# Optimization experiments

Hardware: AMD Instinct MI355X
Metric: run time of the kernel (lower is better)

## Reference

```python
import jax, jax.numpy as jnp
import numpy as np

METRIC_SCALE = 0.01  # metric = I + 0.01 * outer(p, p)


def setup_inputs() -> dict:
    key = jax.random.key(0)
    kq, kk = jax.random.split(key)
    query_points = jax.random.normal(kq, (8192, 512), dtype=jnp.float32)
    key_points = jax.random.normal(kk, (8192, 512), dtype=jnp.float32)
    return {"query_points": query_points, "key_points": key_points}


def reference(query_points, key_points):
    # diff_ij = q_i - k_j;  dist^2 under metric (I + c * p p^T) is
    # ||diff||^2 + c * (p . diff)^2 -- avoids materializing [Nq, Nk, d] diffs.
    c = METRIC_SCALE
    qq = jnp.sum(query_points * query_points, axis=-1)          # [Nq]
    kk = jnp.sum(key_points * key_points, axis=-1)              # [Nk]
    qk = jnp.einsum('qd,kd->qk', query_points, key_points)      # [Nq, Nk]
    norm2 = jnp.maximum(qq[:, None] + kk[None, :] - 2.0 * qk, 0.0)
    qdot = qq[:, None] - qk                                     # q_i . (q_i - k_j)
    kdot = qk - kk[None, :]                                     # k_j . (q_i - k_j) (sign irrelevant, squared)
    query_dist = jnp.sqrt(norm2 + c * qdot * qdot)
    key_dist = jnp.sqrt(norm2 + c * kdot * kdot)
    scores = -0.5 * (query_dist + key_dist)
    return jax.nn.softmax(scores, axis=-1)
```

## Files before the change

### kernel.cpp

```cpp
#include <hip/hip_runtime.h>
#include <stdint.h>


#define NQ 8192
#define NK 8192
#define DIM 512
#define CSCALE 0.01f

typedef float f32x4 __attribute__((ext_vector_type(4)));
typedef short s16x8 __attribute__((ext_vector_type(8)));
typedef unsigned short u16x4 __attribute__((ext_vector_type(4)));

__device__ __forceinline__ unsigned short f2bf(float x) {
  union { float f; uint32_t u; } c; c.f = x;
  uint32_t u = c.u;
  return (unsigned short)((u + 0x7fffu + ((u >> 16) & 1u)) >> 16);
}

__device__ __forceinline__ float bf2f(unsigned short h) {
  union { uint32_t u; float f; } c; c.u = ((uint32_t)h) << 16;
  return c.f;
}

__device__ __forceinline__ s16x8 pack8(f32x4 a, f32x4 b) {
  s16x8 r;
  r[0]=(short)f2bf(a.x); r[1]=(short)f2bf(a.y);
  r[2]=(short)f2bf(a.z); r[3]=(short)f2bf(a.w);
  r[4]=(short)f2bf(b.x); r[5]=(short)f2bf(b.y);
  r[6]=(short)f2bf(b.z); r[7]=(short)f2bf(b.w);
  return r;
}

#define GLOAD_LDS16(g, l)                                                      \
  __builtin_amdgcn_global_load_lds(                                            \
      (const __attribute__((address_space(1))) void*)(g),                      \
      (__attribute__((address_space(3))) void*)(l), 16, 0, 0)

__global__ __launch_bounds__(256) void prep_full_kernel(
    const float* __restrict__ q, const float* __restrict__ k,
    unsigned short* __restrict__ qbf, unsigned short* __restrict__ kbf,
    float* __restrict__ qq, float* __restrict__ kk) {
  int rowg = blockIdx.x * 4 + (threadIdx.x >> 6);
  int lane = threadIdx.x & 63;
  const float* src; unsigned short* dst; float* nrm; int row;
  if (rowg < NQ) { src = q; dst = qbf; nrm = qq; row = rowg; }
  else           { src = k; dst = kbf; nrm = kk; row = rowg - NQ; }
  const float* p = src + (size_t)row * DIM + lane * 8;
  f32x4 a = *(const f32x4*)p;
  f32x4 b = *(const f32x4*)(p + 4);
  float ss = a.x*a.x + a.y*a.y + a.z*a.z + a.w*a.w
           + b.x*b.x + b.y*b.y + b.z*b.z + b.w*b.w;
  *(s16x8*)(dst + (size_t)row * DIM + lane * 8) = pack8(a, b);
#pragma unroll
  for (int mask = 1; mask < 64; mask <<= 1) ss += __shfl_xor(ss, mask, 64);
  if (lane == 0) nrm[row] = ss;
}

__global__ __launch_bounds__(256) void prep_norms_kernel(
    const float* __restrict__ q, const float* __restrict__ k,
    float* __restrict__ qq, float* __restrict__ kk) {
  int rowg = blockIdx.x * 4 + (threadIdx.x >> 6);
  int lane = threadIdx.x & 63;
  const float* src; float* nrm; int row;
  if (rowg < NQ) { src = q; nrm = qq; row = rowg; }
  else           { src = k; nrm = kk; row = rowg - NQ; }
  const float* p = src + (size_t)row * DIM + lane * 8;
  f32x4 a = *(const f32x4*)p;
  f32x4 b = *(const f32x4*)(p + 4);
  float ss = a.x*a.x + a.y*a.y + a.z*a.z + a.w*a.w
           + b.x*b.x + b.y*b.y + b.z*b.z + b.w*b.w;
#pragma unroll
  for (int mask = 1; mask < 64; mask <<= 1) ss += __shfl_xor(ss, mask, 64);
  if (lane == 0) nrm[row] = ss;
}

__device__ __forceinline__ float score_fn(float qkv, float qqv, float kkv) {
  float n2 = fmaxf(qqv + kkv - 2.f * qkv, 0.f);
  float qd = qqv - qkv;
  float kd = qkv - kkv;
  return -0.5f * (__builtin_amdgcn_sqrtf(n2 + CSCALE * qd * qd) +
                  __builtin_amdgcn_sqrtf(n2 + CSCALE * kd * kd));
}

__global__ __launch_bounds__(256) void gemm_exp_kernel(
    const unsigned short* __restrict__ qbf, const unsigned short* __restrict__ kbf,
    const float* __restrict__ qq, const float* __restrict__ kk,
    unsigned short* __restrict__ E) {
  __shared__ alignas(16) unsigned short smem[8192];
  const int tid = threadIdx.x;
  const int m0 = blockIdx.y * 128;
  const int n0 = blockIdx.x * 128;
  const int wave = tid >> 6, lane = tid & 63;
  const int wr = wave >> 1, wc = wave & 1;
  const int quad = lane >> 4, lcol = lane & 15;

  const int srow = tid >> 2;
  const int gsw = (tid & 3) ^ ((srow >> 1) & 3);
  const unsigned short* ga = qbf + (size_t)(m0 + srow) * DIM + gsw * 8;
  const unsigned short* gb = kbf + (size_t)(n0 + srow) * DIM + gsw * 8;
  char* la0 = (char*)smem + wave * 1024;
  char* lb0 = (char*)smem + 8192 + wave * 1024;

  f32x4 acc[4][4];
#pragma unroll
  for (int mi = 0; mi < 4; ++mi)
#pragma unroll
    for (int ni = 0; ni < 4; ++ni) acc[mi][ni] = f32x4{0.f, 0.f, 0.f, 0.f};

  const s16x8* lA8 = (const s16x8*)smem;
  const s16x8* lB8 = (const s16x8*)(smem + 4096);
  const int arow = wr * 64 + lcol;
  const int brow = wc * 64 + lcol;
  const int swz = (lcol >> 1) & 3;
  const int qsw = quad ^ swz;

  for (int kt = 0; kt < DIM / 32; ++kt) {
    const int ko = kt * 32;
    GLOAD_LDS16(ga + ko, la0);
    GLOAD_LDS16(ga + ko + 64 * DIM, la0 + 4096);
    GLOAD_LDS16(gb + ko, lb0);
    GLOAD_LDS16(gb + ko + 64 * DIM, lb0 + 4096);
    __syncthreads();
    s16x8 af[4], bfr[4];
#pragma unroll
    for (int mi = 0; mi < 4; ++mi) af[mi] = lA8[(arow + mi * 16) * 4 + qsw];
#pragma unroll
    for (int ni = 0; ni < 4; ++ni) bfr[ni] = lB8[(brow + ni * 16) * 4 + qsw];
#pragma unroll
    for (int mi = 0; mi < 4; ++mi)
#pragma unroll
      for (int ni = 0; ni < 4; ++ni)
        acc[mi][ni] = __builtin_amdgcn_mfma_f32_16x16x32_bf16(
            af[mi], bfr[ni], acc[mi][ni], 0, 0, 0);
    __syncthreads();
  }

  unsigned short* tw = smem + wave * 1280;
  float kkv[4];
#pragma unroll
  for (int ni = 0; ni < 4; ++ni) kkv[ni] = kk[n0 + wc * 64 + ni * 16 + lcol];
#pragma unroll
  for (int mi = 0; mi < 4; ++mi) {
    const int ibase = m0 + wr * 64 + mi * 16 + quad * 4;
    float qqv[4];
#pragma unroll
    for (int r = 0; r < 4; ++r) qqv[r] = qq[ibase + r];
#pragma unroll
    for (int ni = 0; ni < 4; ++ni)
#pragma unroll
      for (int r = 0; r < 4; ++r) {
        float e = __expf(score_fn(acc[mi][ni][r], qqv[r], kkv[ni]));
        tw[(quad * 4 + r) * 80 + ((ni ^ quad) * 16 + lcol)] = f2bf(e);
      }
#pragma unroll
    for (int j = 0; j < 2; ++j) {
      const int row16 = (lane >> 3) + j * 8;
      const int g = (lane & 7) >> 1;
      const int off = row16 * 80 + ((g ^ (row16 >> 2)) * 16) + (lane & 1) * 8;
      s16x8 vv = *(const s16x8*)(tw + off);
      const int rowg = m0 + wr * 64 + mi * 16 + row16;
      *(s16x8*)(E + (size_t)rowg * NK + n0 + wc * 64 + (lane & 7) * 8) = vv;
    }
  }
}

__global__ __launch_bounds__(256) void rowsum_scale_kernel(
    const unsigned short* __restrict__ E, float* __restrict__ out) {
  __shared__ float red[4];
  const int t = threadIdx.x;
  const int wave = t >> 6, lane = t & 63;
  const unsigned short* Erow = E + (size_t)blockIdx.x * NK;
  float* Orow = out + (size_t)blockIdx.x * NK;
  u16x4 ev[8];
  float s = 0.f;
#pragma unroll
  for (int j = 0; j < 8; ++j) {
    ev[j] = *(const u16x4*)(Erow + j * 1024 + t * 4);
    s += (bf2f(ev[j][0]) + bf2f(ev[j][1])) + (bf2f(ev[j][2]) + bf2f(ev[j][3]));
  }
#pragma unroll
  for (int mask = 1; mask < 64; mask <<= 1) s += __shfl_xor(s, mask, 64);
  if (lane == 0) red[wave] = s;
  __syncthreads();
  float z = 1.0f / ((red[0] + red[1]) + (red[2] + red[3]));
#pragma unroll
  for (int j = 0; j < 8; ++j) {
    f32x4 v;
    v.x = bf2f(ev[j][0]) * z;
    v.y = bf2f(ev[j][1]) * z;
    v.z = bf2f(ev[j][2]) * z;
    v.w = bf2f(ev[j][3]) * z;
    *(f32x4*)(Orow + j * 1024 + t * 4) = v;
  }
}

__device__ __forceinline__ void score_epilogue(
    const f32x4 acc[4][4], const float* __restrict__ qq,
    const float* __restrict__ kk, float* __restrict__ S,
    int m0, int n0, int wr, int wc, int quad, int lcol) {
  float kkv[4];
#pragma unroll
  for (int ni = 0; ni < 4; ++ni) kkv[ni] = kk[n0 + wc * 64 + ni * 16 + lcol];
#pragma unroll
  for (int mi = 0; mi < 4; ++mi) {
    const int ibase = m0 + wr * 64 + mi * 16 + quad * 4;
    float qqv[4];
#pragma unroll
    for (int r = 0; r < 4; ++r) qqv[r] = qq[ibase + r];
#pragma unroll
    for (int ni = 0; ni < 4; ++ni) {
      const int col = n0 + wc * 64 + ni * 16 + lcol;
#pragma unroll
      for (int r = 0; r < 4; ++r)
        S[(size_t)(ibase + r) * NK + col] = score_fn(acc[mi][ni][r], qqv[r], kkv[ni]);
    }
  }
}

__global__ __launch_bounds__(256) void gemm_fast_kernel(
    const unsigned short* __restrict__ qbf, const unsigned short* __restrict__ kbf,
    const float* __restrict__ qq, const float* __restrict__ kk,
    float* __restrict__ S) {
  __shared__ unsigned short lA[128 * 32];
  __shared__ unsigned short lB[128 * 32];
  const int tid = threadIdx.x;
  const int m0 = blockIdx.y * 128;
  const int n0 = blockIdx.x * 128;
  const int wave = tid >> 6, lane = tid & 63;
  const int wr = wave >> 1, wc = wave & 1;
  const int quad = lane >> 4, lcol = lane & 15;
  const unsigned short* ga = qbf + (size_t)(m0 + (tid >> 2)) * DIM + (tid & 3) * 8;
  const unsigned short* gb = kbf + (size_t)(n0 + (tid >> 2)) * DIM + (tid & 3) * 8;
  char* la0 = (char*)lA + wave * 1024;
  char* lb0 = (char*)lB + wave * 1024;
  f32x4 acc[4][4];
#pragma unroll
  for (int mi = 0; mi < 4; ++mi)
#pragma unroll
    for (int ni = 0; ni < 4; ++ni) acc[mi][ni] = f32x4{0.f, 0.f, 0.f, 0.f};
  const s16x8* lA8 = (const s16x8*)lA;
  const s16x8* lB8 = (const s16x8*)lB;
  const int arow = wr * 64 + lcol;
  const int brow = wc * 64 + lcol;
  for (int kt = 0; kt < DIM / 32; ++kt) {
    const int ko = kt * 32;
    GLOAD_LDS16(ga + ko, la0);
    GLOAD_LDS16(ga + ko + 64 * DIM, la0 + 4096);
    GLOAD_LDS16(gb + ko, lb0);
    GLOAD_LDS16(gb + ko + 64 * DIM, lb0 + 4096);
    __syncthreads();
    s16x8 af[4], bfr[4];
#pragma unroll
    for (int mi = 0; mi < 4; ++mi) af[mi] = lA8[(arow + mi * 16) * 4 + quad];
#pragma unroll
    for (int ni = 0; ni < 4; ++ni) bfr[ni] = lB8[(brow + ni * 16) * 4 + quad];
#pragma unroll
    for (int mi = 0; mi < 4; ++mi)
#pragma unroll
      for (int ni = 0; ni < 4; ++ni)
        acc[mi][ni] = __builtin_amdgcn_mfma_f32_16x16x32_bf16(
            af[mi], bfr[ni], acc[mi][ni], 0, 0, 0);
    __syncthreads();
  }
  score_epilogue(acc, qq, kk, S, m0, n0, wr, wc, quad, lcol);
}

__global__ __launch_bounds__(256) void gemm_safe_kernel(
    const float* __restrict__ q, const float* __restrict__ k,
    const float* __restrict__ qq, const float* __restrict__ kk,
    float* __restrict__ S) {
  __shared__ unsigned short lA[128 * 32];
  __shared__ unsigned short lB[128 * 32];
  const int tid = threadIdx.x;
  const int m0 = blockIdx.y * 128;
  const int n0 = blockIdx.x * 128;
  const int wave = tid >> 6, lane = tid & 63;
  const int wr = wave >> 1, wc = wave & 1;
  const int quad = lane >> 4, lcol = lane & 15;
  const float* gaf = q + (size_t)(m0 + (tid >> 1)) * DIM + (tid & 1) * 16;
  const float* gbf = k + (size_t)(n0 + (tid >> 1)) * DIM + (tid & 1) * 16;
  unsigned short* wA = lA + (tid >> 1) * 32 + (tid & 1) * 16;
  unsigned short* wB = lB + (tid >> 1) * 32 + (tid & 1) * 16;
  f32x4 acc[4][4];
#pragma unroll
  for (int mi = 0; mi < 4; ++mi)
#pragma unroll
    for (int ni = 0; ni < 4; ++ni) acc[mi][ni] = f32x4{0.f, 0.f, 0.f, 0.f};
  const s16x8* lA8 = (const s16x8*)lA;
  const s16x8* lB8 = (const s16x8*)lB;
  const int arow = wr * 64 + lcol;
  const int brow = wc * 64 + lcol;
  for (int kt = 0; kt < DIM / 32; ++kt) {
    const float* pa = gaf + kt * 32;
    const float* pb = gbf + kt * 32;
    f32x4 a0 = *(const f32x4*)(pa), a1 = *(const f32x4*)(pa + 4);
    f32x4 a2 = *(const f32x4*)(pa + 8), a3 = *(const f32x4*)(pa + 12);
    f32x4 b0 = *(const f32x4*)(pb), b1 = *(const f32x4*)(pb + 4);
    f32x4 b2 = *(const f32x4*)(pb + 8), b3 = *(const f32x4*)(pb + 12);
    *(s16x8*)wA = pack8(a0, a1);
    *(s16x8*)(wA + 8) = pack8(a2, a3);
    *(s16x8*)wB = pack8(b0, b1);
    *(s16x8*)(wB + 8) = pack8(b2, b3);
    __syncthreads();
    s16x8 af[4], bfr[4];
#pragma unroll
    for (int mi = 0; mi < 4; ++mi) af[mi] = lA8[(arow + mi * 16) * 4 + quad];
#pragma unroll
    for (int ni = 0; ni < 4; ++ni) bfr[ni] = lB8[(brow + ni * 16) * 4 + quad];
#pragma unroll
    for (int mi = 0; mi < 4; ++mi)
#pragma unroll
      for (int ni = 0; ni < 4; ++ni)
        acc[mi][ni] = __builtin_amdgcn_mfma_f32_16x16x32_bf16(
            af[mi], bfr[ni], acc[mi][ni], 0, 0, 0);
    __syncthreads();
  }
  score_epilogue(acc, qq, kk, S, m0, n0, wr, wc, quad, lcol);
}

__global__ __launch_bounds__(256) void rowsoftmax_kernel(float* __restrict__ S) {
  __shared__ float red[8];
  const int t = threadIdx.x;
  const int wave = t >> 6, lane = t & 63;
  float* Srow = S + (size_t)blockIdx.x * NK;
  f32x4 v[8];
  float m = -1e30f;
#pragma unroll
  for (int j = 0; j < 8; ++j) {
    v[j] = *(const f32x4*)(Srow + j * 1024 + t * 4);
    m = fmaxf(m, fmaxf(fmaxf(v[j].x, v[j].y), fmaxf(v[j].z, v[j].w)));
  }
#pragma unroll
  for (int mask = 1; mask < 64; mask <<= 1) m = fmaxf(m, __shfl_xor(m, mask, 64));
  if (lane == 0) red[wave] = m;
  __syncthreads();
  m = fmaxf(fmaxf(red[0], red[1]), fmaxf(red[2], red[3]));
  float s = 0.f;
#pragma unroll
  for (int j = 0; j < 8; ++j) {
    v[j].x = __expf(v[j].x - m);
    v[j].y = __expf(v[j].y - m);
    v[j].z = __expf(v[j].z - m);
    v[j].w = __expf(v[j].w - m);
    s += (v[j].x + v[j].y) + (v[j].z + v[j].w);
  }
#pragma unroll
  for (int mask = 1; mask < 64; mask <<= 1) s += __shfl_xor(s, mask, 64);
  if (lane == 0) red[4 + wave] = s;
  __syncthreads();
  float z = 1.0f / ((red[4] + red[5]) + (red[6] + red[7]));
#pragma unroll
  for (int j = 0; j < 8; ++j) {
    v[j].x *= z; v[j].y *= z; v[j].z *= z; v[j].w *= z;
    *(f32x4*)(Srow + j * 1024 + t * 4) = v[j];
  }
}

extern "C" void kernel_launch(void* const* d_in, const int* in_sizes, int n_in,
                              void* d_out, int out_size, void* d_ws, size_t ws_size,
                              hipStream_t stream) {
  const float* q = (const float*)d_in[0];
  const float* k = (const float*)d_in[1];
  float* S = (float*)d_out;
  char* ws = (char*)d_ws;

  if (ws_size >= (size_t)151126016) {
    unsigned short* qbf = (unsigned short*)(ws);
    unsigned short* kbf = (unsigned short*)(ws + 8388608);
    float* qq = (float*)(ws + 16777216);
    float* kk = (float*)(ws + 16777216 + 32768);
    unsigned short* E = (unsigned short*)(ws + 16908288);
    prep_full_kernel<<<4096, 256, 0, stream>>>(q, k, qbf, kbf, qq, kk);
    gemm_exp_kernel<<<dim3(64, 64), 256, 0, stream>>>(qbf, kbf, qq, kk, E);
    rowsum_scale_kernel<<<NQ, 256, 0, stream>>>(E, S);
  } else if (ws_size >= (size_t)16842752) {
    unsigned short* qbf = (unsigned short*)(ws);
    unsigned short* kbf = (unsigned short*)(ws + 8388608);
    float* qq = (float*)(ws + 16777216);
    float* kk = (float*)(ws + 16777216 + 32768);
    prep_full_kernel<<<4096, 256, 0, stream>>>(q, k, qbf, kbf, qq, kk);
    gemm_fast_kernel<<<dim3(64, 64), 256, 0, stream>>>(qbf, kbf, qq, kk, S);
    rowsoftmax_kernel<<<NQ, 256, 0, stream>>>(S);
  } else {
    float* qq = (float*)(ws);
    float* kk = (float*)(ws + 32768);
    prep_norms_kernel<<<4096, 256, 0, stream>>>(q, k, qq, kk);
    gemm_safe_kernel<<<dim3(64, 64), 256, 0, stream>>>(q, k, qq, kk, S);
    rowsoftmax_kernel<<<NQ, 256, 0, stream>>>(S);
  }
}
```

Measured before the change: 428.3 us.

## Double-buffer GEMM LDS tiles and widen rowsum loads to 16 bytes

The GEMM main loop now uses two LDS buffers, so the next K tile is loaded directly into LDS while MFMAs run on the current one. This replaces the two barriers per tile with one waitcnt plus barrier, and doubles LDS use to 32KB per block. The softmax normalization kernel now reads eight bf16 values per thread with 16-byte loads instead of four, which halves the number of load instructions. The larger LDS footprint may lower occupancy.

```diff
diff --git a/kernel.cpp b/kernel.cpp
--- a/kernel.cpp
+++ b/kernel.cpp
@@ -86,7 +86,7 @@
     const unsigned short* __restrict__ qbf, const unsigned short* __restrict__ kbf,
     const float* __restrict__ qq, const float* __restrict__ kk,
     unsigned short* __restrict__ E) {
-  __shared__ alignas(16) unsigned short smem[8192];
+  __shared__ alignas(16) unsigned short smem[16384];
   const int tid = threadIdx.x;
   const int m0 = blockIdx.y * 128;
   const int n0 = blockIdx.x * 128;
@@ -98,8 +98,8 @@
   const int gsw = (tid & 3) ^ ((srow >> 1) & 3);
   const unsigned short* ga = qbf + (size_t)(m0 + srow) * DIM + gsw * 8;
   const unsigned short* gb = kbf + (size_t)(n0 + srow) * DIM + gsw * 8;
-  char* la0 = (char*)smem + wave * 1024;
-  char* lb0 = (char*)smem + 8192 + wave * 1024;
+  char* labase = (char*)smem;
+  const int stageoff = wave * 1024;
 
   f32x4 acc[4][4];
 #pragma unroll
@@ -107,33 +107,58 @@
 #pragma unroll
     for (int ni = 0; ni < 4; ++ni) acc[mi][ni] = f32x4{0.f, 0.f, 0.f, 0.f};
 
-  const s16x8* lA8 = (const s16x8*)smem;
-  const s16x8* lB8 = (const s16x8*)(smem + 4096);
   const int arow = wr * 64 + lcol;
   const int brow = wc * 64 + lcol;
   const int swz = (lcol >> 1) & 3;
   const int qsw = quad ^ swz;
 
-  for (int kt = 0; kt < DIM / 32; ++kt) {
-    const int ko = kt * 32;
-    GLOAD_LDS16(ga + ko, la0);
-    GLOAD_LDS16(ga + ko + 64 * DIM, la0 + 4096);
-    GLOAD_LDS16(gb + ko, lb0);
-    GLOAD_LDS16(gb + ko + 64 * DIM, lb0 + 4096);
-    __syncthreads();
-    s16x8 af[4], bfr[4];
-#pragma unroll
-    for (int mi = 0; mi < 4; ++mi) af[mi] = lA8[(arow + mi * 16) * 4 + qsw];
-#pragma unroll
-    for (int ni = 0; ni < 4; ++ni) bfr[ni] = lB8[(brow + ni * 16) * 4 + qsw];
-#pragma unroll
-    for (int mi = 0; mi < 4; ++mi)
-#pragma unroll
-      for (int ni = 0; ni < 4; ++ni)
-        acc[mi][ni] = __builtin_amdgcn_mfma_f32_16x16x32_bf16(
-            af[mi], bfr[ni], acc[mi][ni], 0, 0, 0);
-    __syncthreads();
-  }
+#define STAGE_TILE(bufbyte, ko)                                                \
+  do {                                                                         \
+    GLOAD_LDS16(ga + (ko), labase + (bufbyte) + stageoff);                     \
+    GLOAD_LDS16(ga + (ko) + 64 * DIM, labase + (bufbyte) + stageoff + 4096);   \
+    GLOAD_LDS16(gb + (ko), labase + (bufbyte) + 8192 + stageoff);              \
+    GLOAD_LDS16(gb + (ko) + 64 * DIM,                                          \
+                labase + (bufbyte) + 8192 + stageoff + 4096);                  \
+  } while (0)
+
+#define COMPUTE_TILE(bufbyte)                                                  \
+  do {                                                                         \
+    const s16x8* lA8 = (const s16x8*)(labase + (bufbyte));                     \
+    const s16x8* lB8 = (const s16x8*)(labase + (bufbyte) + 8192);              \
+    s16x8 af[4], bfr[4];                                                       \
+    _Pragma("unroll")                                                          \
+    for (int mi = 0; mi < 4; ++mi) af[mi] = lA8[(arow + mi * 16) * 4 + qsw];   \
+    _Pragma("unroll")                                                          \
+    for (int ni = 0; ni < 4; ++ni) bfr[ni] = lB8[(brow + ni * 16) * 4 + qsw];  \
+    _Pragma("unroll")                                                          \
+    for (int mi = 0; mi < 4; ++mi)                                             \
+      _Pragma("unroll")                                                        \
+      for (int ni = 0; ni < 4; ++ni)                                           \
+        acc[mi][ni] = __builtin_amdgcn_mfma_f32_16x16x32_bf16(                 \
+            af[mi], bfr[ni], acc[mi][ni], 0, 0, 0);                            \
+  } while (0)
+
+#define SYNC_PIPE()                                                            \
+  do {                                                                         \
+    asm volatile("s_waitcnt vmcnt(0)" ::: "memory");                           \
+    __builtin_amdgcn_s_barrier();                                              \
+  } while (0)
+
+  const int NT = DIM / 32;
+  STAGE_TILE(0, 0);
+  SYNC_PIPE();
+#pragma unroll 1
+  for (int kt = 0; kt < NT; kt += 2) {
+    STAGE_TILE(16384, (kt + 1) * 32);
+    COMPUTE_TILE(0);
+    SYNC_PIPE();
+    if (kt + 2 < NT) STAGE_TILE(0, (kt + 2) * 32);
+    COMPUTE_TILE(16384);
+    SYNC_PIPE();
+  }
+#undef STAGE_TILE
+#undef COMPUTE_TILE
+#undef SYNC_PIPE
 
   unsigned short* tw = smem + wave * 1280;
   float kkv[4];
@@ -171,12 +196,16 @@
   const int wave = t >> 6, lane = t & 63;
   const unsigned short* Erow = E + (size_t)blockIdx.x * NK;
   float* Orow = out + (size_t)blockIdx.x * NK;
-  u16x4 ev[8];
+  s16x8 ev[4];
   float s = 0.f;
 #pragma unroll
-  for (int j = 0; j < 8; ++j) {
-    ev[j] = *(const u16x4*)(Erow + j * 1024 + t * 4);
-    s += (bf2f(ev[j][0]) + bf2f(ev[j][1])) + (bf2f(ev[j][2]) + bf2f(ev[j][3]));
+  for (int j = 0; j < 4; ++j) {
+    ev[j] = *(const s16x8*)(Erow + j * 2048 + t * 8);
+    float a0 = bf2f((unsigned short)ev[j][0]) + bf2f((unsigned short)ev[j][1]);
+    float a1 = bf2f((unsigned short)ev[j][2]) + bf2f((unsigned short)ev[j][3]);
+    float a2 = bf2f((unsigned short)ev[j][4]) + bf2f((unsigned short)ev[j][5]);
+    float a3 = bf2f((unsigned short)ev[j][6]) + bf2f((unsigned short)ev[j][7]);
+    s += (a0 + a1) + (a2 + a3);
   }
 #pragma unroll
   for (int mask = 1; mask < 64; mask <<= 1) s += __shfl_xor(s, mask, 64);
@@ -184,13 +213,18 @@
   __syncthreads();
   float z = 1.0f / ((red[0] + red[1]) + (red[2] + red[3]));
 #pragma unroll
-  for (int j = 0; j < 8; ++j) {
-    f32x4 v;
-    v.x = bf2f(ev[j][0]) * z;
-    v.y = bf2f(ev[j][1]) * z;
-    v.z = bf2f(ev[j][2]) * z;
-    v.w = bf2f(ev[j][3]) * z;
-    *(f32x4*)(Orow + j * 1024 + t * 4) = v;
+  for (int j = 0; j < 4; ++j) {
+    f32x4 lo, hi;
+    lo.x = bf2f((unsigned short)ev[j][0]) * z;
+    lo.y = bf2f((unsigned short)ev[j][1]) * z;
+    lo.z = bf2f((unsigned short)ev[j][2]) * z;
+    lo.w = bf2f((unsigned short)ev[j][3]) * z;
+    hi.x = bf2f((unsigned short)ev[j][4]) * z;
+    hi.y = bf2f((unsigned short)ev[j][5]) * z;
+    hi.z = bf2f((unsigned short)ev[j][6]) * z;
+    hi.w = bf2f((unsigned short)ev[j][7]) * z;
+    *(f32x4*)(Orow + j * 2048 + t * 8) = lo;
+    *(f32x4*)(Orow + j * 2048 + t * 8 + 4) = hi;
   }
 }
 
```

Result: no change. 432.1 us (+0.9%).
